# Optimization experiments

Hardware: AMD Instinct MI355X
Metric: run time of the kernel (lower is better)

## Reference

```python
import jax, jax.numpy as jnp
import numpy as np
import math

# ---- static config (matches init_kwargs) ----
B, L, CIN = 16, 192, 21
D = 128          # d_model
LAYERS = 2
P, S = 24, 12    # patch_length, stride
PRED, COUT = 96, 21
BN_EPS = 1e-5
NT = L // S      # number of patches = 16


def _conv1d(x, w, b=None, stride=1, padding=0):
    # x: (N, Cin, L), w: (Cout, Cin, K)
    y = jax.lax.conv_general_dilated(x, w, (stride,), [(padding, padding)],
                                     dimension_numbers=("NCH", "OIH", "NCH"))
    if b is not None:
        y = y + b[None, :, None]
    return y


def _conv2d(x, w, padding):
    # x: (N, Cin, H, W), w: (Cout, Cin, kh, kw)
    return jax.lax.conv_general_dilated(x, w, (1, 1), padding,
                                        dimension_numbers=("NCHW", "OIHW", "NCHW"))


def _pos_embed(length, d):
    pos = jnp.arange(length, dtype=jnp.float32)[:, None]
    div = jnp.exp(jnp.arange(0, d, 2, dtype=jnp.float32) * (-math.log(10000.0) / d))
    pe = jnp.zeros((length, d), jnp.float32)
    pe = pe.at[:, 0::2].set(jnp.sin(pos * div)).at[:, 1::2].set(jnp.cos(pos * div))
    return pe


def _times_block(x, Wi, pw, pb, g, beta, aw):
    # x: (b, c, t, h, w); Wi: (out=c, in=c, 3, 3)
    b, c, t, h, w = x.shape
    res = x
    pp = x.mean(axis=(3, 4))                       # AdaptiveAvgPool3d((None,1,1)) -> (b,c,t)
    pp = _conv1d(pp, pw, pb, padding=1)            # period_conv
    scale = g / jnp.sqrt(1.0 + BN_EPS)             # eval-mode BN, running stats (0, 1)
    pp = jax.nn.relu(pp * scale[None, :, None] + beta[None, :, None])
    pooled = pp.mean(axis=-1)                      # AdaptiveAvgPool1d(1) -> (b,c)
    alpha = jnp.einsum("oc,bc->bo", aw, pooled) + 1.0   # alpha_conv (1x1, no bias) + 1
    # dynamic weight: (b, out, in, 3, 3) -> (b*out, in, 3, 3)
    Wd = (Wi[None] * alpha[:, :, None, None, None]).reshape(b * c, c, 3, 3)
    x2 = x.reshape(b, c, t, h * w)
    # conv2d with groups=1: every sample sees ALL b*out filters -> (b, b*out, t-2, hw-2)
    y = _conv2d(x2, Wd, [(0, 0), (0, 0)])
    # conv_transpose2d(y, Wd) == conv2d(y, flip(Wd).swap(O,I), full padding)
    Wt = jnp.swapaxes(jnp.flip(Wd, (-2, -1)), 0, 1)     # (c, b*out, 3, 3)
    z = _conv2d(y, Wt, [(2, 2), (2, 2)])                 # (b, c, t, hw)
    return z.reshape(b, c, t, h, w) + res


def setup_inputs() -> dict:
    key = jax.random.key(0)
    ks = jax.random.split(key, 13)
    rn = lambda k, shp, s: jax.random.normal(k, shp, jnp.float32) * s
    return {
        "x": jax.random.normal(ks[0], (B, L, CIN), jnp.float32),
        "token_w": rn(ks[1], (D, CIN, 3), 1.0 / np.sqrt(CIN * 3)),
        "patch_w": rn(ks[2], (P, 1, P), 1.0 / np.sqrt(P)),
        "patch_b": rn(ks[3], (P,), 0.02),
        "Wi": rn(ks[4], (LAYERS, D, D, 3, 3), 1.0 / np.sqrt(D * 9)),
        "pconv_w": rn(ks[5], (LAYERS, D, D, 3), 1.0 / np.sqrt(D * 3)),
        "pconv_b": rn(ks[6], (LAYERS, D), 0.02),
        "bn_g": jnp.ones((LAYERS, D), jnp.float32),
        "bn_b": jnp.zeros((LAYERS, D), jnp.float32),
        "aconv_w": rn(ks[7], (LAYERS, D, D), 1.0 / np.sqrt(D)),
        "fc1_w": rn(ks[8], (PRED, 2 * L), 1.0 / np.sqrt(2 * L)),
        "fc1_b": rn(ks[9], (PRED,), 0.02),
        "fc2_w": rn(ks[10], (COUT, D), 1.0 / np.sqrt(D)),
        "fc2_b": rn(ks[11], (COUT,), 0.02),
    }


def reference(x, token_w, patch_w, patch_b, Wi, pconv_w, pconv_b,
              bn_g, bn_b, aconv_w, fc1_w, fc1_b, fc2_w, fc2_b):
    # ---- DataEmbedding (dropout in eval mode) ----
    xt = jnp.pad(x.transpose(0, 2, 1), ((0, 0), (0, 0), (1, 1)), mode="wrap")  # circular pad
    emb = _conv1d(xt, token_w).transpose(0, 2, 1)            # (B, L, D)
    emb = emb + _pos_embed(L, D)[None]
    # ---- patch Embedding ----
    xe = emb.reshape(B * D, 1, L)                             # matches torch reshape/permute
    xe = jnp.pad(xe, ((0, 0), (0, 0), (0, P - S)), mode="edge")  # replicate pad
    xe = _conv1d(xe, patch_w, patch_b, stride=S)              # (B*D, P, NT)
    xe = xe.transpose(0, 2, 1).reshape(B, NT, P, D)           # torch reshape semantics (C-order)
    x5 = jnp.stack([xe[:, :, 0::2, :], xe[:, :, 1::2, :]], axis=2)  # (B, NT, 2, P//2, D)
    x5 = x5.transpose(0, 4, 1, 2, 3)                          # (B, D, NT, 2, 12)
    # ---- TimesBlocks ----
    for i in range(LAYERS):
        x5 = _times_block(x5, Wi[i], pconv_w[i], pconv_b[i], bn_g[i], bn_b[i], aconv_w[i])
    # ---- heads ----
    xf = x5.reshape(B, -1, D)                                 # (B, 2L, D)
    y1 = xf.transpose(0, 2, 1) @ fc1_w.T + fc1_b              # (B, D, PRED)
    out = y1.transpose(0, 2, 1) @ fc2_w.T + fc2_b             # (B, PRED, COUT)
    return out
```

## Files before the change

kernel.cpp:

```cpp
#include <hip/hip_runtime.h>
#include <math.h>

constexpr int cB = 16, cL = 192, cCIN = 21, cD = 128;
constexpr int cNT = 16, cHW = 24;
constexpr int cPRED = 96, cCOUT = 21;
constexpr int cYH = 14, cYW = 22;

typedef __attribute__((ext_vector_type(8))) short bf16x8;
typedef __attribute__((ext_vector_type(4))) float f32x4;

__device__ inline unsigned short f2bf(float f) {
    union { float f; unsigned u; } v; v.f = f;
    unsigned u = v.u;
    unsigned r = (u + 0x7fffu + ((u >> 16) & 1u)) >> 16;
    return (unsigned short)r;
}

__device__ inline f32x4 mfma16(bf16x8 a, bf16x8 b, f32x4 c) {
    return __builtin_amdgcn_mfma_f32_16x16x32_bf16(a, b, c, 0, 0, 0);
}

__global__ void k_init(const float* __restrict__ Wi, const float* __restrict__ fc1_w,
                       const float* __restrict__ token_w, const float* __restrict__ fc2_w,
                       unsigned short* __restrict__ Wp, unsigned short* __restrict__ w1p,
                       float* __restrict__ twT, unsigned short* __restrict__ w2p,
                       float* __restrict__ w2s, float* __restrict__ peT,
                       unsigned short* __restrict__ Y0T) {
    int e = blockIdx.x * blockDim.x + threadIdx.x;
    if (e < 589824) {
        int lyr = e / 294912;
        int rem = e % 294912;
        int dir = rem / 147456;
        int q = rem % 147456;
        int kt = q >> 12;
        int oi = (q >> 9) & 7;
        int kg = (q >> 7) & 3;
        int r  = (q >> 3) & 15;
        int j  = q & 7;
        int k = kt * 32 + kg * 8 + j;
        int a = k >> 7;
        int o, c;
        if (dir == 0) { o = oi * 16 + r; c = k & 127; }
        else          { o = k & 127;     c = oi * 16 + r; }
        Wp[e] = f2bf(Wi[lyr * 147456 + o * 1152 + c * 9 + a]);
        return;
    }
    e -= 589824;
    if (e < 36864) {
        int p = e / 384, mh = e % 384;
        w1p[e] = f2bf(fc1_w[p * 384 + 3 * (mh & 127) + (mh >> 7)]);
        return;
    }
    e -= 36864;
    if (e < 8064) {
        int d = e & 127, c3 = e >> 7;
        twT[e] = token_w[d * 63 + c3];
        return;
    }
    e -= 8064;
    if (e < 4096) {
        int q = e >> 7, d = e & 127;
        w2p[e] = (q < 21) ? f2bf(fc2_w[q * 128 + d]) : (unsigned short)0;
        return;
    }
    e -= 4096;
    if (e < 32) {
        if (e < 21) {
            float s = 0.f;
            for (int d = 0; d < 128; ++d) s += fc2_w[e * 128 + d];
            w2s[e] = s;
        } else if (e < 32) w2s[e] = 0.f;
        return;
    }
    e -= 32;
    if (e < 24576) {
        int l = e >> 7, d = e & 127;
        int i2 = d >> 1;
        float dv = expf(-(float)(2 * i2) * (9.210340371976184f / 128.f));
        float ang = (float)l * dv;
        peT[e] = (d & 1) ? cosf(ang) : sinf(ang);
        return;
    }
    e -= 24576;
    if (e < 16384) {
        int n = e >> 10, j = e & 1023;
        bf16x8 z = {0, 0, 0, 0, 0, 0, 0, 0};
        *(bf16x8*)(Y0T + n * 65536 + j * 8) = z;
    }
}

__global__ void k_embed(const float* __restrict__ x, const float* __restrict__ twT,
                        const float* __restrict__ peT, float* __restrict__ emb) {
    int idx = blockIdx.x * blockDim.x + threadIdx.x;
    if (idx >= cB * cL * cD) return;
    int d = idx & 127;
    int r = idx >> 7;
    int l = r % cL;
    int b = r / cL;
    int lm = (l == 0) ? 191 : l - 1;
    int lp = (l == 191) ? 0 : l + 1;
    const float* xb = x + b * 4032;
    float acc = peT[l * 128 + d];
    for (int c = 0; c < cCIN; ++c) {
        float x0 = xb[lm * 21 + c], x1 = xb[l * 21 + c], x2 = xb[lp * 21 + c];
        const float* tb = twT + c * 384 + d;
        acc += x0 * tb[0] + x1 * tb[128] + x2 * tb[256];
    }
    emb[idx] = acc;
}

__global__ __launch_bounds__(192) void k_patch(const float* __restrict__ emb,
                                               const float* __restrict__ pw,
                                               const float* __restrict__ pb,
                                               float* __restrict__ x5) {
    __shared__ float pwL[24][24];
    int t = threadIdx.x;
    for (int z = t; z < 576; z += 192) pwL[z / 24][z % 24] = pw[z];
    __syncthreads();
    int pair = blockIdx.x * 8 + t / 24;
    int p = t % 24;
    int i = pair >> 4, tt = pair & 15;
    const float* ebase = emb + i * 192;
    int j0 = tt * 12;
    float acc = pb[p];
    #pragma unroll
    for (int k = 0; k < 24; ++k) {
        int j = j0 + k;
        j = j > 191 ? 191 : j;
        acc += ebase[j] * pwL[p][k];
    }
    int G = (i & 127) * 384 + tt * 24 + p;
    int b = i >> 7;
    int tp = G / 3072;
    int pp2 = (G % 3072) / 128;
    int cc = G & 127;
    x5[b * 49152 + cc * 384 + tp * 24 + (pp2 & 1) * 12 + (pp2 >> 1)] = acc;
}

__global__ __launch_bounds__(256) void k_stats(const float* __restrict__ x5,
        const float* __restrict__ pw, const float* __restrict__ pb,
        const float* __restrict__ g, const float* __restrict__ bb,
        const float* __restrict__ aw, float* __restrict__ alpha,
        unsigned short* __restrict__ XT, int pack) {
    __shared__ float ppT[18][128];
    __shared__ float part[256];
    __shared__ float pooled[128];
    __shared__ unsigned short tile[64][136];
    int b = blockIdx.x, t = threadIdx.x;
    if (t < 128) { ppT[0][t] = 0.f; ppT[17][t] = 0.f; }
    #pragma unroll
    for (int i = 0; i < 8; ++i) {
        int ct = t + 256 * i;
        const float* p = x5 + b * 49152 + ct * 24;
        float s = 0.f;
        #pragma unroll
        for (int j = 0; j < 6; ++j) {
            f32x4 v = *(const f32x4*)(p + 4 * j);
            s += v[0] + v[1] + v[2] + v[3];
        }
        ppT[1 + (ct & 15)][ct >> 4] = s * (1.f / 24.f);
    }
    __syncthreads();
    int o = t >> 1, th = (t & 1) * 8;
    float acc[8];
    float pbo = pb[o];
    #pragma unroll
    for (int i = 0; i < 8; ++i) acc[i] = pbo;
    for (int c4 = 0; c4 < 32; ++c4) {
        union { f32x4 v[3]; float f[12]; } u;
        u.v[0] = *(const f32x4*)(pw + o * 384 + c4 * 12);
        u.v[1] = *(const f32x4*)(pw + o * 384 + c4 * 12 + 4);
        u.v[2] = *(const f32x4*)(pw + o * 384 + c4 * 12 + 8);
        f32x4 pv[10];
        #pragma unroll
        for (int r = 0; r < 10; ++r) pv[r] = *(f32x4*)&ppT[th + r][c4 * 4];
        #pragma unroll
        for (int cc = 0; cc < 4; ++cc) {
            float a0 = u.f[cc * 3], a1 = u.f[cc * 3 + 1], a2 = u.f[cc * 3 + 2];
            #pragma unroll
            for (int i = 0; i < 8; ++i)
                acc[i] += a0 * pv[i][cc] + a1 * pv[i + 1][cc] + a2 * pv[i + 2][cc];
        }
    }
    float scale = g[o] * rsqrtf(1.f + 1e-5f);
    float beta = bb[o];
    float partial = 0.f;
    #pragma unroll
    for (int i = 0; i < 8; ++i) {
        float v = acc[i] * scale + beta;
        partial += v > 0.f ? v : 0.f;
    }
    part[t] = partial;
    __syncthreads();
    if (t < 128) pooled[t] = (part[2 * t] + part[2 * t + 1]) * (1.f / 16.f);
    __syncthreads();
    if (t < 128) {
        float a = 1.f;
        for (int c4 = 0; c4 < 32; ++c4) {
            f32x4 av = *(const f32x4*)(aw + t * 128 + c4 * 4);
            f32x4 pv4 = *(f32x4*)&pooled[c4 * 4];
            a += av[0] * pv4[0] + av[1] * pv4[1] + av[2] * pv4[2] + av[3] * pv4[3];
        }
        alpha[b * 128 + t] = a;
    }
    if (!pack) return;
    for (int ch = 0; ch < 6; ++ch) {
        __syncthreads();
        int p4 = (t & 15) * 4;
        #pragma unroll
        for (int i = 0; i < 8; ++i) {
            int c = (t >> 4) + i * 16;
            f32x4 v = *(const f32x4*)(x5 + b * 49152 + c * 384 + ch * 64 + p4);
            #pragma unroll
            for (int r = 0; r < 4; ++r) tile[p4 + r][c] = f2bf(v[r]);
        }
        __syncthreads();
        #pragma unroll
        for (int i = 0; i < 4; ++i) {
            int idx = t + i * 256;
            int pp = idx >> 4, c8 = (idx & 15) * 8;
            *(bf16x8*)(XT + b * 57344 + (ch * 64 + pp) * 128 + c8) = *(bf16x8*)&tile[pp][c8];
        }
    }
    bf16x8 z = {0, 0, 0, 0, 0, 0, 0, 0};
    #pragma unroll
    for (int i = 0; i < 4; ++i) {
        int idx = t + i * 256;
        int pp = idx >> 4, c8 = (idx & 15) * 8;
        *(bf16x8*)(XT + b * 57344 + (384 + pp) * 128 + c8) = z;
    }
}

__global__ __launch_bounds__(64) void k_gfwd(const unsigned short* __restrict__ XT,
        const unsigned short* __restrict__ Wp, const float* __restrict__ alpha,
        unsigned short* __restrict__ Y0T) {
    int bid = blockIdx.x;
    int rm = bid >> 1, cn = bid & 1;
    int n = rm / 12, p0 = (rm % 12) * 32;
    int o0 = cn * 64;
    int l = threadIdx.x;
    int sm = l & 15, skg = l >> 4;
    const unsigned short* XTn = XT + n * 57344;
    const unsigned short* WB = Wp + (o0 >> 4) * 512 + l * 8;
    f32x4 acc[2][4];
    #pragma unroll
    for (int mi = 0; mi < 2; ++mi)
        #pragma unroll
        for (int ni = 0; ni < 4; ++ni) acc[mi][ni] = (f32x4){0.f, 0.f, 0.f, 0.f};
    #pragma unroll
    for (int kt = 0; kt < 36; ++kt) {
        int a = kt >> 2;
        int off = (a / 3) * 24 + (a % 3);
        int kc = (kt & 3) * 32 + skg * 8;
        const unsigned short* ab = XTn + (p0 + sm + off) * 128 + kc;
        bf16x8 a0 = *(const bf16x8*)(ab);
        bf16x8 a1 = *(const bf16x8*)(ab + 2048);
        const unsigned short* wb = WB + kt * 4096;
        bf16x8 b0 = *(const bf16x8*)(wb);
        bf16x8 b1 = *(const bf16x8*)(wb + 512);
        bf16x8 b2 = *(const bf16x8*)(wb + 1024);
        bf16x8 b3 = *(const bf16x8*)(wb + 1536);
        acc[0][0] = mfma16(a0, b0, acc[0][0]);
        acc[0][1] = mfma16(a0, b1, acc[0][1]);
        acc[0][2] = mfma16(a0, b2, acc[0][2]);
        acc[0][3] = mfma16(a0, b3, acc[0][3]);
        acc[1][0] = mfma16(a1, b0, acc[1][0]);
        acc[1][1] = mfma16(a1, b1, acc[1][1]);
        acc[1][2] = mfma16(a1, b2, acc[1][2]);
        acc[1][3] = mfma16(a1, b3, acc[1][3]);
    }
    #pragma unroll
    for (int ni = 0; ni < 4; ++ni) {
        int o = o0 + ni * 16 + sm;
        float s = 0.f;
        #pragma unroll
        for (int bb2 = 0; bb2 < 16; ++bb2) { float a = alpha[bb2 * 128 + o]; s += a * a; }
        #pragma unroll
        for (int mi = 0; mi < 2; ++mi) {
            #pragma unroll
            for (int r = 0; r < 4; ++r) {
                int p = p0 + mi * 16 + skg * 4 + r;
                bool valid = ((p % 24) < cYW) && ((p / 24) < cYH);
                float v = valid ? acc[mi][ni][r] * s : 0.f;
                Y0T[n * 65536 + (64 + p) * 128 + o] = f2bf(v);
            }
        }
    }
}

__global__ __launch_bounds__(64) void k_gbwd(const unsigned short* __restrict__ Y0T,
        const unsigned short* __restrict__ Wpb, float* __restrict__ x5,
        unsigned short* __restrict__ xdst, int mode) {
    __shared__ unsigned short tr[32][72];
    int bid = blockIdx.x;
    int rm = bid >> 1, cn = bid & 1;
    int n = rm / 12, p0 = (rm % 12) * 32;
    int c0 = cn * 64;
    int l = threadIdx.x;
    int sm = l & 15, skg = l >> 4;
    const unsigned short* Yn = Y0T + n * 65536 + 64 * 128;
    const unsigned short* WB = Wpb + (c0 >> 4) * 512 + l * 8;
    f32x4 acc[2][4];
    #pragma unroll
    for (int mi = 0; mi < 2; ++mi)
        #pragma unroll
        for (int ni = 0; ni < 4; ++ni) acc[mi][ni] = (f32x4){0.f, 0.f, 0.f, 0.f};
    #pragma unroll
    for (int kt = 0; kt < 36; ++kt) {
        int a = kt >> 2;
        int off = (a / 3) * 24 + (a % 3);
        int kc = (kt & 3) * 32 + skg * 8;
        const unsigned short* ab = Yn + (p0 + sm - off) * 128 + kc;
        bf16x8 a0 = *(const bf16x8*)(ab);
        bf16x8 a1 = *(const bf16x8*)(ab + 2048);
        const unsigned short* wb = WB + kt * 4096;
        bf16x8 b0 = *(const bf16x8*)(wb);
        bf16x8 b1 = *(const bf16x8*)(wb + 512);
        bf16x8 b2 = *(const bf16x8*)(wb + 1024);
        bf16x8 b3 = *(const bf16x8*)(wb + 1536);
        acc[0][0] = mfma16(a0, b0, acc[0][0]);
        acc[0][1] = mfma16(a0, b1, acc[0][1]);
        acc[0][2] = mfma16(a0, b2, acc[0][2]);
        acc[0][3] = mfma16(a0, b3, acc[0][3]);
        acc[1][0] = mfma16(a1, b0, acc[1][0]);
        acc[1][1] = mfma16(a1, b1, acc[1][1]);
        acc[1][2] = mfma16(a1, b2, acc[1][2]);
        acc[1][3] = mfma16(a1, b3, acc[1][3]);
    }
    #pragma unroll
    for (int ni = 0; ni < 4; ++ni) {
        int cl = ni * 16 + sm;
        int c = c0 + cl;
        #pragma unroll
        for (int mi = 0; mi < 2; ++mi) {
            int pl = mi * 16 + skg * 4;
            float* dst = x5 + n * 49152 + c * 384 + p0 + pl;
            f32x4 ov = *(f32x4*)dst;
            #pragma unroll
            for (int r = 0; r < 4; ++r) {
                ov[r] += acc[mi][ni][r];
                tr[pl + r][cl] = f2bf(ov[r]);
            }
            *(f32x4*)dst = ov;
        }
    }
    __syncthreads();
    if (mode == 0) {
        #pragma unroll
        for (int pass = 0; pass < 4; ++pass) {
            int idx = pass * 64 + l;
            int row = idx >> 3, ch = idx & 7;
            *(bf16x8*)(xdst + n * 57344 + (p0 + row) * 128 + c0 + ch * 8) = *(bf16x8*)&tr[row][ch * 8];
        }
    } else {
        #pragma unroll
        for (int pass = 0; pass < 4; ++pass) {
            int idx = pass * 64 + l;
            int cl = idx >> 2, pl0 = (idx & 3) * 8;
            __attribute__((aligned(16))) unsigned short tmp[8];
            #pragma unroll
            for (int j2 = 0; j2 < 8; ++j2) tmp[j2] = tr[pl0 + j2][cl];
            *(bf16x8*)(xdst + n * 49152 + ((p0 >> 7) * 128 + c0 + cl) * 128 + (p0 & 127) + pl0) =
                *(bf16x8*)tmp;
        }
    }
}

__global__ __launch_bounds__(64) void k_gemmZ(const unsigned short* __restrict__ xfM,
        const unsigned short* __restrict__ w2p, unsigned short* __restrict__ Zt) {
    int bid = blockIdx.x;
    int b = bid / 12, m0 = (bid % 12) * 32;
    int l = threadIdx.x, sm = l & 15, skg = l >> 4;
    f32x4 acc[2][2];
    #pragma unroll
    for (int mi = 0; mi < 2; ++mi)
        #pragma unroll
        for (int ni = 0; ni < 2; ++ni) acc[mi][ni] = (f32x4){0.f, 0.f, 0.f, 0.f};
    #pragma unroll
    for (int kt = 0; kt < 4; ++kt) {
        int kc = kt * 32 + skg * 8;
        const unsigned short* ab = xfM + b * 49152 + (m0 + sm) * 128 + kc;
        bf16x8 a0 = *(const bf16x8*)(ab);
        bf16x8 a1 = *(const bf16x8*)(ab + 2048);
        bf16x8 b0 = *(const bf16x8*)(w2p + sm * 128 + kc);
        bf16x8 b1 = *(const bf16x8*)(w2p + (16 + sm) * 128 + kc);
        acc[0][0] = mfma16(a0, b0, acc[0][0]);
        acc[0][1] = mfma16(a0, b1, acc[0][1]);
        acc[1][0] = mfma16(a1, b0, acc[1][0]);
        acc[1][1] = mfma16(a1, b1, acc[1][1]);
    }
    #pragma unroll
    for (int mi = 0; mi < 2; ++mi)
        #pragma unroll
        for (int ni = 0; ni < 2; ++ni) {
            int q = ni * 16 + sm;
            int mh = m0 + mi * 16 + skg * 4;
            #pragma unroll
            for (int r = 0; r < 4; ++r)
                Zt[b * 12288 + q * 384 + mh + r] = f2bf(acc[mi][ni][r]);
        }
}

__global__ __launch_bounds__(64) void k_gemmO(const unsigned short* __restrict__ w1p,
        const unsigned short* __restrict__ Zt, const float* __restrict__ b1,
        const float* __restrict__ w2s, const float* __restrict__ b2,
        float* __restrict__ out) {
    int bid = blockIdx.x;
    int b = bid / 3, p0 = (bid % 3) * 32;
    int l = threadIdx.x, sm = l & 15, skg = l >> 4;
    f32x4 acc[2][2];
    #pragma unroll
    for (int mi = 0; mi < 2; ++mi)
        #pragma unroll
        for (int ni = 0; ni < 2; ++ni) acc[mi][ni] = (f32x4){0.f, 0.f, 0.f, 0.f};
    #pragma unroll
    for (int kt = 0; kt < 12; ++kt) {
        int kc = kt * 32 + skg * 8;
        const unsigned short* ab = w1p + (p0 + sm) * 384 + kc;
        bf16x8 a0 = *(const bf16x8*)(ab);
        bf16x8 a1 = *(const bf16x8*)(ab + 16 * 384);
        const unsigned short* zb = Zt + b * 12288 + sm * 384 + kc;
        bf16x8 b0 = *(const bf16x8*)(zb);
        bf16x8 b1v = *(const bf16x8*)(zb + 16 * 384);
        acc[0][0] = mfma16(a0, b0, acc[0][0]);
        acc[0][1] = mfma16(a0, b1v, acc[0][1]);
        acc[1][0] = mfma16(a1, b0, acc[1][0]);
        acc[1][1] = mfma16(a1, b1v, acc[1][1]);
    }
    #pragma unroll
    for (int ni = 0; ni < 2; ++ni) {
        int q = ni * 16 + sm;
        if (q < 21) {
            float wsq = w2s[q], bq = b2[q];
            #pragma unroll
            for (int mi = 0; mi < 2; ++mi) {
                #pragma unroll
                for (int r = 0; r < 4; ++r) {
                    int p = p0 + mi * 16 + skg * 4 + r;
                    out[b * 2016 + p * 21 + q] = acc[mi][ni][r] + b1[p] * wsq + bq;
                }
            }
        }
    }
}

extern "C" void kernel_launch(void* const* d_in, const int* in_sizes, int n_in,
                              void* d_out, int out_size, void* d_ws, size_t ws_size,
                              hipStream_t stream) {
    const float* x       = (const float*)d_in[0];
    const float* token_w = (const float*)d_in[1];
    const float* patch_w = (const float*)d_in[2];
    const float* patch_b = (const float*)d_in[3];
    const float* Wi      = (const float*)d_in[4];
    const float* pconv_w = (const float*)d_in[5];
    const float* pconv_b = (const float*)d_in[6];
    const float* bn_g    = (const float*)d_in[7];
    const float* bn_b    = (const float*)d_in[8];
    const float* aconv_w = (const float*)d_in[9];
    const float* fc1_w   = (const float*)d_in[10];
    const float* fc1_b   = (const float*)d_in[11];
    const float* fc2_w   = (const float*)d_in[12];
    const float* fc2_b   = (const float*)d_in[13];
    float* out = (float*)d_out;

    float* ws    = (float*)d_ws;
    float* x5    = ws;
    float* alpha = ws + 786432;
    unsigned short* Wp  = (unsigned short*)(ws + 788480);
    unsigned short* w1p = (unsigned short*)(ws + 1083392);
    unsigned short* w2p = (unsigned short*)(ws + 1101824);
    float* w2s   = ws + 1103872;
    float* twT   = ws + 1103904;
    float* peT   = ws + 1111968;
    float* emb   = ws + 1136544;
    unsigned short* XT  = (unsigned short*)(ws + 1136544 + 393216);
    unsigned short* xfM = XT;
    unsigned short* Y0T = (unsigned short*)(ws + 1136544 + 393216 + 458752);
    unsigned short* Zt  = Y0T;

    k_init<<<2656, 256, 0, stream>>>(Wi, fc1_w, token_w, fc2_w, Wp, w1p, twT, w2p, w2s, peT, Y0T);
    k_embed<<<1536, 256, 0, stream>>>(x, twT, peT, emb);
    k_patch<<<4096, 192, 0, stream>>>(emb, patch_w, patch_b, x5);
    k_stats<<<16, 256, 0, stream>>>(x5, pconv_w, pconv_b, bn_g, bn_b, aconv_w, alpha, XT, 1);
    k_gfwd<<<384, 64, 0, stream>>>(XT, Wp, alpha, Y0T);
    k_gbwd<<<384, 64, 0, stream>>>(Y0T, Wp + 147456, x5, XT, 0);
    k_stats<<<16, 256, 0, stream>>>(x5, pconv_w + 49152, pconv_b + 128, bn_g + 128,
                                    bn_b + 128, aconv_w + 16384, alpha, XT, 0);
    k_gfwd<<<384, 64, 0, stream>>>(XT, Wp + 2 * 147456, alpha, Y0T);
    k_gbwd<<<384, 64, 0, stream>>>(Y0T, Wp + 3 * 147456, x5, xfM, 1);
    k_gemmZ<<<192, 64, 0, stream>>>(xfM, w2p, Zt);
    k_gemmO<<<48, 64, 0, stream>>>(w1p, Zt, fc1_b, w2s, fc2_b, out);
}
```

Before: 230.1 us.

## Fuse init, embedding, patching and XT packing; merge head GEMMs into one kernel

```diff
diff --git a/kernel.cpp b/kernel.cpp
--- a/kernel.cpp
+++ b/kernel.cpp
@@ -1,9 +1,7 @@
 #include <hip/hip_runtime.h>
 #include <math.h>
 
-constexpr int cB = 16, cL = 192, cCIN = 21, cD = 128;
-constexpr int cNT = 16, cHW = 24;
-constexpr int cPRED = 96, cCOUT = 21;
+constexpr int cCIN = 21;
 constexpr int cYH = 14, cYW = 22;
 
 typedef __attribute__((ext_vector_type(8))) short bf16x8;
@@ -20,145 +18,152 @@
     return __builtin_amdgcn_mfma_f32_16x16x32_bf16(a, b, c, 0, 0, 0);
 }
 
-__global__ void k_init(const float* __restrict__ Wi, const float* __restrict__ fc1_w,
-                       const float* __restrict__ token_w, const float* __restrict__ fc2_w,
-                       unsigned short* __restrict__ Wp, unsigned short* __restrict__ w1p,
-                       float* __restrict__ twT, unsigned short* __restrict__ w2p,
-                       float* __restrict__ w2s, float* __restrict__ peT,
-                       unsigned short* __restrict__ Y0T) {
-    int e = blockIdx.x * blockDim.x + threadIdx.x;
-    if (e < 589824) {
-        int lyr = e / 294912;
-        int rem = e % 294912;
-        int dir = rem / 147456;
-        int q = rem % 147456;
-        int kt = q >> 12;
-        int oi = (q >> 9) & 7;
-        int kg = (q >> 7) & 3;
-        int r  = (q >> 3) & 15;
-        int j  = q & 7;
-        int k = kt * 32 + kg * 8 + j;
-        int a = k >> 7;
-        int o, c;
-        if (dir == 0) { o = oi * 16 + r; c = k & 127; }
-        else          { o = k & 127;     c = oi * 16 + r; }
-        Wp[e] = f2bf(Wi[lyr * 147456 + o * 1152 + c * 9 + a]);
+__global__ __launch_bounds__(256) void k_initep(
+        const float* __restrict__ x, const float* __restrict__ token_w,
+        const float* __restrict__ patch_w, const float* __restrict__ patch_b,
+        const float* __restrict__ Wi, const float* __restrict__ fc1_w,
+        const float* __restrict__ fc2_w,
+        float* __restrict__ x5, unsigned short* __restrict__ XT,
+        unsigned short* __restrict__ Wp, unsigned short* __restrict__ w1p,
+        unsigned short* __restrict__ w2p, float* __restrict__ w2s,
+        unsigned short* __restrict__ Y0T) {
+    __shared__ float twL[8064];
+    __shared__ float embL[1536];
+    __shared__ float pwL[576];
+    int t = threadIdx.x;
+    if (blockIdx.x < 256) {
+        int blk = blockIdx.x;
+        for (int z = t; z < 8064; z += 256) {
+            int d = z & 127, c3 = z >> 7;
+            twL[z] = token_w[d * 63 + c3];
+        }
+        for (int z = t; z < 576; z += 256) pwL[z] = patch_w[z];
+        __syncthreads();
+        int b = blk >> 4;
+        const float* xb = x + b * 4032;
+        #pragma unroll
+        for (int pass = 0; pass < 6; ++pass) {
+            int v = t + pass * 256;
+            int f = blk * 1536 + v;
+            int ll = (f % 24576) / 128;
+            int d = f & 127;
+            int lm = (ll == 0) ? 191 : ll - 1;
+            int lp = (ll == 191) ? 0 : ll + 1;
+            int i2 = d >> 1;
+            float dv = expf(-(float)(2 * i2) * (9.210340371976184f / 128.f));
+            float ang = (float)ll * dv;
+            float acc = (d & 1) ? cosf(ang) : sinf(ang);
+            for (int c = 0; c < cCIN; ++c) {
+                float x0 = xb[lm * 21 + c], x1 = xb[ll * 21 + c], x2 = xb[lp * 21 + c];
+                acc += x0 * twL[(c * 3 + 0) * 128 + d]
+                     + x1 * twL[(c * 3 + 1) * 128 + d]
+                     + x2 * twL[(c * 3 + 2) * 128 + d];
+            }
+            embL[v] = acc;
+        }
+        __syncthreads();
+        #pragma unroll
+        for (int pass = 0; pass < 12; ++pass) {
+            int u = t + pass * 256;
+            int ri = u / 384, rem = u % 384, tt = rem / 24, p = rem % 24;
+            int i = blk * 8 + ri;
+            int j0 = tt * 12;
+            float acc = patch_b[p];
+            #pragma unroll
+            for (int k = 0; k < 24; ++k) {
+                int j = j0 + k;
+                j = j > 191 ? 191 : j;
+                acc += embL[ri * 192 + j] * pwL[p * 24 + k];
+            }
+            int G = (i & 127) * 384 + tt * 24 + p;
+            int b2 = i >> 7;
+            int tp = G / 3072;
+            int pp2 = (G % 3072) / 128;
+            int cc = G & 127;
+            int pp = tp * 24 + (pp2 & 1) * 12 + (pp2 >> 1);
+            x5[b2 * 49152 + cc * 384 + pp] = acc;
+            XT[b2 * 57344 + pp * 128 + cc] = f2bf(acc);
+        }
         return;
     }
-    e -= 589824;
-    if (e < 36864) {
-        int p = e / 384, mh = e % 384;
-        w1p[e] = f2bf(fc1_w[p * 384 + 3 * (mh & 127) + (mh >> 7)]);
-        return;
-    }
-    e -= 36864;
-    if (e < 8064) {
-        int d = e & 127, c3 = e >> 7;
-        twT[e] = token_w[d * 63 + c3];
-        return;
-    }
-    e -= 8064;
-    if (e < 4096) {
-        int q = e >> 7, d = e & 127;
-        w2p[e] = (q < 21) ? f2bf(fc2_w[q * 128 + d]) : (unsigned short)0;
-        return;
-    }
-    e -= 4096;
-    if (e < 32) {
-        if (e < 21) {
-            float s = 0.f;
-            for (int d = 0; d < 128; ++d) s += fc2_w[e * 128 + d];
-            w2s[e] = s;
-        } else if (e < 32) w2s[e] = 0.f;
-        return;
-    }
-    e -= 32;
-    if (e < 24576) {
-        int l = e >> 7, d = e & 127;
-        int i2 = d >> 1;
-        float dv = expf(-(float)(2 * i2) * (9.210340371976184f / 128.f));
-        float ang = (float)l * dv;
-        peT[e] = (d & 1) ? cosf(ang) : sinf(ang);
-        return;
-    }
-    e -= 24576;
-    if (e < 16384) {
-        int n = e >> 10, j = e & 1023;
-        bf16x8 z = {0, 0, 0, 0, 0, 0, 0, 0};
-        *(bf16x8*)(Y0T + n * 65536 + j * 8) = z;
-    }
-}
-
-__global__ void k_embed(const float* __restrict__ x, const float* __restrict__ twT,
-                        const float* __restrict__ peT, float* __restrict__ emb) {
-    int idx = blockIdx.x * blockDim.x + threadIdx.x;
-    if (idx >= cB * cL * cD) return;
-    int d = idx & 127;
-    int r = idx >> 7;
-    int l = r % cL;
-    int b = r / cL;
-    int lm = (l == 0) ? 191 : l - 1;
-    int lp = (l == 191) ? 0 : l + 1;
-    const float* xb = x + b * 4032;
-    float acc = peT[l * 128 + d];
-    for (int c = 0; c < cCIN; ++c) {
-        float x0 = xb[lm * 21 + c], x1 = xb[l * 21 + c], x2 = xb[lp * 21 + c];
-        const float* tb = twT + c * 384 + d;
-        acc += x0 * tb[0] + x1 * tb[128] + x2 * tb[256];
-    }
-    emb[idx] = acc;
-}
-
-__global__ __launch_bounds__(192) void k_patch(const float* __restrict__ emb,
-                                               const float* __restrict__ pw,
-                                               const float* __restrict__ pb,
-                                               float* __restrict__ x5) {
-    __shared__ float pwL[24][24];
-    int t = threadIdx.x;
-    for (int z = t; z < 576; z += 192) pwL[z / 24][z % 24] = pw[z];
-    __syncthreads();
-    int pair = blockIdx.x * 8 + t / 24;
-    int p = t % 24;
-    int i = pair >> 4, tt = pair & 15;
-    const float* ebase = emb + i * 192;
-    int j0 = tt * 12;
-    float acc = pb[p];
-    #pragma unroll
-    for (int k = 0; k < 24; ++k) {
-        int j = j0 + k;
-        j = j > 191 ? 191 : j;
-        acc += ebase[j] * pwL[p][k];
-    }
-    int G = (i & 127) * 384 + tt * 24 + p;
-    int b = i >> 7;
-    int tp = G / 3072;
-    int pp2 = (G % 3072) / 128;
-    int cc = G & 127;
-    x5[b * 49152 + cc * 384 + tp * 24 + (pp2 & 1) * 12 + (pp2 >> 1)] = acc;
+    for (int e0 = (blockIdx.x - 256) * 256 + t; e0 < 663584; e0 += 512 * 256) {
+        int e = e0;
+        if (e < 589824) {
+            int lyr = e / 294912;
+            int rem = e % 294912;
+            int dir = rem / 147456;
+            int q = rem % 147456;
+            int kt = q >> 12;
+            int oi = (q >> 9) & 7;
+            int kg = (q >> 7) & 3;
+            int r  = (q >> 3) & 15;
+            int j  = q & 7;
+            int k = kt * 32 + kg * 8 + j;
+            int a = k >> 7;
+            int o, c;
+            if (dir == 0) { o = oi * 16 + r; c = k & 127; }
+            else          { o = k & 127;     c = oi * 16 + r; }
+            Wp[e] = f2bf(Wi[lyr * 147456 + o * 1152 + c * 9 + a]);
+            continue;
+        }
+        e -= 589824;
+        if (e < 36864) {
+            int p = e / 384, mh = e % 384;
+            w1p[e] = f2bf(fc1_w[p * 384 + 3 * (mh & 127) + (mh >> 7)]);
+            continue;
+        }
+        e -= 36864;
+        if (e < 4096) {
+            int q = e >> 7, d = e & 127;
+            w2p[e] = (q < 21) ? f2bf(fc2_w[q * 128 + d]) : (unsigned short)0;
+            continue;
+        }
+        e -= 4096;
+        if (e < 32) {
+            if (e < 21) {
+                float ssum = 0.f;
+                for (int d = 0; d < 128; ++d) ssum += fc2_w[e * 128 + d];
+                w2s[e] = ssum;
+            } else w2s[e] = 0.f;
+            continue;
+        }
+        e -= 32;
+        if (e < 16384) {
+            int n = e >> 10, rem2 = e & 1023;
+            int pp = 384 + (rem2 >> 4), c8 = (rem2 & 15) * 8;
+            bf16x8 z = {0, 0, 0, 0, 0, 0, 0, 0};
+            *(bf16x8*)(XT + n * 57344 + pp * 128 + c8) = z;
+            continue;
+        }
+        e -= 16384;
+        {
+            int n = e >> 10, j = e & 1023;
+            bf16x8 z = {0, 0, 0, 0, 0, 0, 0, 0};
+            *(bf16x8*)(Y0T + n * 65536 + j * 8) = z;
+        }
+    }
 }
 
 __global__ __launch_bounds__(256) void k_stats(const float* __restrict__ x5,
         const float* __restrict__ pw, const float* __restrict__ pb,
         const float* __restrict__ g, const float* __restrict__ bb,
-        const float* __restrict__ aw, float* __restrict__ alpha,
-        unsigned short* __restrict__ XT, int pack) {
+        const float* __restrict__ aw, float* __restrict__ alpha) {
     __shared__ float ppT[18][128];
     __shared__ float part[256];
     __shared__ float pooled[128];
-    __shared__ unsigned short tile[64][136];
     int b = blockIdx.x, t = threadIdx.x;
     if (t < 128) { ppT[0][t] = 0.f; ppT[17][t] = 0.f; }
     #pragma unroll
     for (int i = 0; i < 8; ++i) {
         int ct = t + 256 * i;
         const float* p = x5 + b * 49152 + ct * 24;
-        float s = 0.f;
+        float ssum = 0.f;
         #pragma unroll
         for (int j = 0; j < 6; ++j) {
             f32x4 v = *(const f32x4*)(p + 4 * j);
-            s += v[0] + v[1] + v[2] + v[3];
-        }
-        ppT[1 + (ct & 15)][ct >> 4] = s * (1.f / 24.f);
+            ssum += v[0] + v[1] + v[2] + v[3];
+        }
+        ppT[1 + (ct & 15)][ct >> 4] = ssum * (1.f / 24.f);
     }
     __syncthreads();
     int o = t >> 1, th = (t & 1) * 8;
@@ -202,32 +207,6 @@
             a += av[0] * pv4[0] + av[1] * pv4[1] + av[2] * pv4[2] + av[3] * pv4[3];
         }
         alpha[b * 128 + t] = a;
-    }
-    if (!pack) return;
-    for (int ch = 0; ch < 6; ++ch) {
-        __syncthreads();
-        int p4 = (t & 15) * 4;
-        #pragma unroll
-        for (int i = 0; i < 8; ++i) {
-            int c = (t >> 4) + i * 16;
-            f32x4 v = *(const f32x4*)(x5 + b * 49152 + c * 384 + ch * 64 + p4);
-            #pragma unroll
-            for (int r = 0; r < 4; ++r) tile[p4 + r][c] = f2bf(v[r]);
-        }
-        __syncthreads();
-        #pragma unroll
-        for (int i = 0; i < 4; ++i) {
-            int idx = t + i * 256;
-            int pp = idx >> 4, c8 = (idx & 15) * 8;
-            *(bf16x8*)(XT + b * 57344 + (ch * 64 + pp) * 128 + c8) = *(bf16x8*)&tile[pp][c8];
-        }
-    }
-    bf16x8 z = {0, 0, 0, 0, 0, 0, 0, 0};
-    #pragma unroll
-    for (int i = 0; i < 4; ++i) {
-        int idx = t + i * 256;
-        int pp = idx >> 4, c8 = (idx & 15) * 8;
-        *(bf16x8*)(XT + b * 57344 + (384 + pp) * 128 + c8) = z;
     }
 }
 
@@ -366,78 +345,78 @@
     }
 }
 
-__global__ __launch_bounds__(64) void k_gemmZ(const unsigned short* __restrict__ xfM,
-        const unsigned short* __restrict__ w2p, unsigned short* __restrict__ Zt) {
-    int bid = blockIdx.x;
-    int b = bid / 12, m0 = (bid % 12) * 32;
-    int l = threadIdx.x, sm = l & 15, skg = l >> 4;
-    f32x4 acc[2][2];
-    #pragma unroll
-    for (int mi = 0; mi < 2; ++mi)
-        #pragma unroll
-        for (int ni = 0; ni < 2; ++ni) acc[mi][ni] = (f32x4){0.f, 0.f, 0.f, 0.f};
-    #pragma unroll
-    for (int kt = 0; kt < 4; ++kt) {
-        int kc = kt * 32 + skg * 8;
-        const unsigned short* ab = xfM + b * 49152 + (m0 + sm) * 128 + kc;
-        bf16x8 a0 = *(const bf16x8*)(ab);
-        bf16x8 a1 = *(const bf16x8*)(ab + 2048);
-        bf16x8 b0 = *(const bf16x8*)(w2p + sm * 128 + kc);
-        bf16x8 b1 = *(const bf16x8*)(w2p + (16 + sm) * 128 + kc);
-        acc[0][0] = mfma16(a0, b0, acc[0][0]);
-        acc[0][1] = mfma16(a0, b1, acc[0][1]);
-        acc[1][0] = mfma16(a1, b0, acc[1][0]);
-        acc[1][1] = mfma16(a1, b1, acc[1][1]);
-    }
-    #pragma unroll
-    for (int mi = 0; mi < 2; ++mi)
+__global__ __launch_bounds__(256) void k_head(const unsigned short* __restrict__ xfM,
+        const unsigned short* __restrict__ w2p, const unsigned short* __restrict__ w1p,
+        const float* __restrict__ b1, const float* __restrict__ w2s,
+        const float* __restrict__ b2, float* __restrict__ out) {
+    __shared__ unsigned short ZtL[12288];
+    int b = blockIdx.x, t = threadIdx.x;
+    int w = t >> 6, l = t & 63;
+    int sm = l & 15, skg = l >> 4;
+    for (int zu = w; zu < 12; zu += 4) {
+        int m0 = zu * 32;
+        f32x4 acc[2][2];
+        #pragma unroll
+        for (int mi = 0; mi < 2; ++mi)
+            #pragma unroll
+            for (int ni = 0; ni < 2; ++ni) acc[mi][ni] = (f32x4){0.f, 0.f, 0.f, 0.f};
+        #pragma unroll
+        for (int kt = 0; kt < 4; ++kt) {
+            int kc = kt * 32 + skg * 8;
+            const unsigned short* ab = xfM + b * 49152 + (m0 + sm) * 128 + kc;
+            bf16x8 a0 = *(const bf16x8*)(ab);
+            bf16x8 a1 = *(const bf16x8*)(ab + 2048);
+            bf16x8 b0 = *(const bf16x8*)(w2p + sm * 128 + kc);
+            bf16x8 b1 = *(const bf16x8*)(w2p + (16 + sm) * 128 + kc);
+            acc[0][0] = mfma16(a0, b0, acc[0][0]);
+            acc[0][1] = mfma16(a0, b1, acc[0][1]);
+            acc[1][0] = mfma16(a1, b0, acc[1][0]);
+            acc[1][1] = mfma16(a1, b1, acc[1][1]);
+        }
+        #pragma unroll
+        for (int mi = 0; mi < 2; ++mi)
+            #pragma unroll
+            for (int ni = 0; ni < 2; ++ni) {
+                int q = ni * 16 + sm;
+                int mh = m0 + mi * 16 + skg * 4;
+                #pragma unroll
+                for (int r = 0; r < 4; ++r)
+                    ZtL[q * 384 + mh + r] = f2bf(acc[mi][ni][r]);
+            }
+    }
+    __syncthreads();
+    if (w < 3) {
+        int p0 = w * 32;
+        f32x4 acc[2][2];
+        #pragma unroll
+        for (int mi = 0; mi < 2; ++mi)
+            #pragma unroll
+            for (int ni = 0; ni < 2; ++ni) acc[mi][ni] = (f32x4){0.f, 0.f, 0.f, 0.f};
+        #pragma unroll
+        for (int kt = 0; kt < 12; ++kt) {
+            int kc = kt * 32 + skg * 8;
+            const unsigned short* ab = w1p + (p0 + sm) * 384 + kc;
+            bf16x8 a0 = *(const bf16x8*)(ab);
+            bf16x8 a1 = *(const bf16x8*)(ab + 16 * 384);
+            bf16x8 b0 = *(const bf16x8*)(&ZtL[sm * 384 + kc]);
+            bf16x8 b1v = *(const bf16x8*)(&ZtL[(16 + sm) * 384 + kc]);
+            acc[0][0] = mfma16(a0, b0, acc[0][0]);
+            acc[0][1] = mfma16(a0, b1v, acc[0][1]);
+            acc[1][0] = mfma16(a1, b0, acc[1][0]);
+            acc[1][1] = mfma16(a1, b1v, acc[1][1]);
+        }
         #pragma unroll
         for (int ni = 0; ni < 2; ++ni) {
             int q = ni * 16 + sm;
-            int mh = m0 + mi * 16 + skg * 4;
-            #pragma unroll
-            for (int r = 0; r < 4; ++r)
-                Zt[b * 12288 + q * 384 + mh + r] = f2bf(acc[mi][ni][r]);
-        }
-}
-
-__global__ __launch_bounds__(64) void k_gemmO(const unsigned short* __restrict__ w1p,
-        const unsigned short* __restrict__ Zt, const float* __restrict__ b1,
-        const float* __restrict__ w2s, const float* __restrict__ b2,
-        float* __restrict__ out) {
-    int bid = blockIdx.x;
-    int b = bid / 3, p0 = (bid % 3) * 32;
-    int l = threadIdx.x, sm = l & 15, skg = l >> 4;
-    f32x4 acc[2][2];
-    #pragma unroll
-    for (int mi = 0; mi < 2; ++mi)
-        #pragma unroll
-        for (int ni = 0; ni < 2; ++ni) acc[mi][ni] = (f32x4){0.f, 0.f, 0.f, 0.f};
-    #pragma unroll
-    for (int kt = 0; kt < 12; ++kt) {
-        int kc = kt * 32 + skg * 8;
-        const unsigned short* ab = w1p + (p0 + sm) * 384 + kc;
-        bf16x8 a0 = *(const bf16x8*)(ab);
-        bf16x8 a1 = *(const bf16x8*)(ab + 16 * 384);
-        const unsigned short* zb = Zt + b * 12288 + sm * 384 + kc;
-        bf16x8 b0 = *(const bf16x8*)(zb);
-        bf16x8 b1v = *(const bf16x8*)(zb + 16 * 384);
-        acc[0][0] = mfma16(a0, b0, acc[0][0]);
-        acc[0][1] = mfma16(a0, b1v, acc[0][1]);
-        acc[1][0] = mfma16(a1, b0, acc[1][0]);
-        acc[1][1] = mfma16(a1, b1v, acc[1][1]);
-    }
-    #pragma unroll
-    for (int ni = 0; ni < 2; ++ni) {
-        int q = ni * 16 + sm;
-        if (q < 21) {
-            float wsq = w2s[q], bq = b2[q];
-            #pragma unroll
-            for (int mi = 0; mi < 2; ++mi) {
+            if (q < 21) {
+                float wsq = w2s[q], bq = b2[q];
                 #pragma unroll
-                for (int r = 0; r < 4; ++r) {
-                    int p = p0 + mi * 16 + skg * 4 + r;
-                    out[b * 2016 + p * 21 + q] = acc[mi][ni][r] + b1[p] * wsq + bq;
+                for (int mi = 0; mi < 2; ++mi) {
+                    #pragma unroll
+                    for (int r = 0; r < 4; ++r) {
+                        int p = p0 + mi * 16 + skg * 4 + r;
+                        out[b * 2016 + p * 21 + q] = acc[mi][ni][r] + b1[p] * wsq + bq;
+                    }
                 }
             }
         }
@@ -470,24 +449,17 @@
     unsigned short* w1p = (unsigned short*)(ws + 1083392);
     unsigned short* w2p = (unsigned short*)(ws + 1101824);
     float* w2s   = ws + 1103872;
-    float* twT   = ws + 1103904;
-    float* peT   = ws + 1111968;
-    float* emb   = ws + 1136544;
-    unsigned short* XT  = (unsigned short*)(ws + 1136544 + 393216);
-    unsigned short* xfM = XT;
-    unsigned short* Y0T = (unsigned short*)(ws + 1136544 + 393216 + 458752);
-    unsigned short* Zt  = Y0T;
-
-    k_init<<<2656, 256, 0, stream>>>(Wi, fc1_w, token_w, fc2_w, Wp, w1p, twT, w2p, w2s, peT, Y0T);
-    k_embed<<<1536, 256, 0, stream>>>(x, twT, peT, emb);
-    k_patch<<<4096, 192, 0, stream>>>(emb, patch_w, patch_b, x5);
-    k_stats<<<16, 256, 0, stream>>>(x5, pconv_w, pconv_b, bn_g, bn_b, aconv_w, alpha, XT, 1);
+    unsigned short* XT  = (unsigned short*)(ws + 1103904);
+    unsigned short* Y0T = (unsigned short*)(ws + 1562656);
+
+    k_initep<<<768, 256, 0, stream>>>(x, token_w, patch_w, patch_b, Wi, fc1_w, fc2_w,
+                                      x5, XT, Wp, w1p, w2p, w2s, Y0T);
+    k_stats<<<16, 256, 0, stream>>>(x5, pconv_w, pconv_b, bn_g, bn_b, aconv_w, alpha);
     k_gfwd<<<384, 64, 0, stream>>>(XT, Wp, alpha, Y0T);
     k_gbwd<<<384, 64, 0, stream>>>(Y0T, Wp + 147456, x5, XT, 0);
     k_stats<<<16, 256, 0, stream>>>(x5, pconv_w + 49152, pconv_b + 128, bn_g + 128,
-                                    bn_b + 128, aconv_w + 16384, alpha, XT, 0);
-    k_gfwd<<<384, 64, 0, stream>>>(XT, Wp + 2 * 147456, alpha, Y0T);
-    k_gbwd<<<384, 64, 0, stream>>>(Y0T, Wp + 3 * 147456, x5, xfM, 1);
-    k_gemmZ<<<192, 64, 0, stream>>>(xfM, w2p, Zt);
-    k_gemmO<<<48, 64, 0, stream>>>(w1p, Zt, fc1_b, w2s, fc2_b, out);
-}
+                                    bn_b + 128, aconv_w + 16384, alpha);
+    k_gfwd<<<384, 64, 0, stream>>>(XT, Wp + 294912, alpha, Y0T);
+    k_gbwd<<<384, 64, 0, stream>>>(Y0T, Wp + 442368, x5, XT , 1);
+    k_head<<<16, 256, 0, stream>>>(XT , w2p, w1p, fc1_b, w2s, fc2_b, out);
+}
```

New measurement: 220.9 us. 4.0% less time.
